# Performance work log

Hardware: AMD Instinct MI355X
Metric: run time of the kernel (lower is better)

## Reference

```python
import jax, jax.numpy as jnp
import numpy as np

BATCH, SEQ, DIM = 8, 2048, 512
NUM_Q, CODEBOOK = 8, 1024


def setup_inputs() -> dict:
    key = jax.random.key(0)
    k1, k2 = jax.random.split(key)
    x = jax.random.normal(k1, (BATCH, SEQ, DIM), dtype=jnp.float32)
    # one codebook per quantizer (uniform codebook size -> stacked [q, c, d])
    codebooks = jax.random.normal(k2, (NUM_Q, CODEBOOK, DIM), dtype=jnp.float32)
    return {"x": x, "codebooks": codebooks}


def reference(x, codebooks):
    """Residual VQ (Algorithm 1, SoundStream). Sequential nearest-neighbor
    quantization of the residual with straight-through estimator.
    project_in/project_out are Identity (codebook_dim == dim).
    Returns (quantized_out [b,n,d], indices [b,n,q], commit_losses [q]).
    """
    residual = x
    quantized_out = jnp.zeros_like(x)
    all_indices = []
    all_losses = []
    num_q = codebooks.shape[0]
    for q in range(num_q):  # small fixed loop over quantizer layers
        cb = codebooks[q]  # [c, d]
        # argmin of squared euclidean distance; ||r||^2 is constant over codes
        scores = -2.0 * jnp.einsum('bnd,cd->bnc', residual, cb) \
                 + jnp.sum(cb * cb, axis=-1)  # [b, n, c]
        idx = jnp.argmin(scores, axis=-1)  # [b, n]
        quant = cb[idx]  # gather codes: [b, n, d]
        # commitment loss (mse of detached quantize vs layer input)
        commit = jnp.mean((jax.lax.stop_gradient(quant) - residual) ** 2)
        # straight-through estimator
        quant_st = residual + jax.lax.stop_gradient(quant - residual)
        quantized_out = quantized_out + quant_st
        residual = residual - jax.lax.stop_gradient(quant)
        all_indices.append(idx)
        all_losses.append(commit)
    indices = jnp.stack(all_indices, axis=-1)  # [b, n, q]
    losses = jnp.stack(all_losses)  # [q]
    return quantized_out, indices, losses
```

## Files before the change

kernel.cpp:

```cpp
#include <hip/hip_runtime.h>
#include <cstdint>
#include <cstddef>


#define BATCH 8
#define SEQ   2048
#define DIM   512
#define NUMQ  8
#define CODES 1024
#define NPTS  (BATCH*SEQ)
#define MPTS  64
#define NWG   (NPTS/MPTS)
#define NTHR  512
#define NCHUNK 32
#define CHUNK_BYTES 32768

#define OUT_IDX   (BATCH*SEQ*DIM)
#define OUT_LOSS  (OUT_IDX + BATCH*SEQ*NUMQ)

#define WS_LOSS   0
#define WS_CNORM  1024
#define WS_CBH    40960
#define WS_CNORMD (WS_CBH + NUMQ*NCHUNK*CHUNK_BYTES)

typedef _Float16 f16x8  __attribute__((ext_vector_type(8)));
typedef _Float16 f16x4  __attribute__((ext_vector_type(4)));
typedef float    f32x16 __attribute__((ext_vector_type(16)));

__global__ void k_zero(double* loss) {
  if (threadIdx.x < NUMQ) loss[threadIdx.x] = 0.0;
}

__global__ void k_cnorm(const float* __restrict__ cb, float* __restrict__ cnorm) {
  int r = blockIdx.x * blockDim.x + threadIdx.x;
  const float* row = cb + (size_t)r * DIM;
  float s = 0.f;
  for (int d = 0; d < DIM; d += 4) {
    float4 v = *(const float4*)(row + d);
    s += v.x * v.x + v.y * v.y + v.z * v.z + v.w * v.w;
  }
  cnorm[r] = s;
}

__global__ void k_cnormd(const float* __restrict__ cb, double* __restrict__ cnd) {
  int r = blockIdx.x * blockDim.x + threadIdx.x;
  const float4* row = (const float4*)(cb + (size_t)r * DIM);
  double d0 = 0, d1 = 0, d2 = 0, d3 = 0;
  for (int i = 0; i < 128; i += 4) {
    float4 a = row[i], b = row[i + 1], c = row[i + 2], d = row[i + 3];
    d0 += (double)a.x * a.x + (double)a.y * a.y + (double)a.z * a.z + (double)a.w * a.w;
    d1 += (double)b.x * b.x + (double)b.y * b.y + (double)b.z * b.z + (double)b.w * b.w;
    d2 += (double)c.x * c.x + (double)c.y * c.y + (double)c.z * c.z + (double)c.w * c.w;
    d3 += (double)d.x * d.x + (double)d.y * d.y + (double)d.z * d.z + (double)d.w * d.w;
  }
  cnd[r] = (d0 + d1) + (d2 + d3);
}

__global__ void k_prep(const float* __restrict__ cb, unsigned char* __restrict__ cbH) {
  unsigned u = blockIdx.x * blockDim.x + threadIdx.x;
  unsigned h  = u & 1;
  unsigned v  = u >> 1;
  unsigned c  = v & 127;
  unsigned g  = (v >> 7) & 1;
  unsigned w  = (v >> 8) & 7;
  unsigned ks = (v >> 11) & 31;
  unsigned q  = v >> 16;
  unsigned code = (w << 7) | c;
  unsigned k = ks * 16 + g * 8 + h * 4;
  float4 val = *(const float4*)(cb + ((size_t)((q << 10) | code)) * DIM + k);
  f16x4 o;
  o[0] = (_Float16)val.x; o[1] = (_Float16)val.y;
  o[2] = (_Float16)val.z; o[3] = (_Float16)val.w;
  *(f16x4*)(cbH + (size_t)u * 8) = o;
}

struct BF { f16x8 b0, b1, b2, b3; };
__device__ __forceinline__ BF loadB(const unsigned char* __restrict__ p) {
  BF r;
  r.b0 = *(const f16x8*)(p);
  r.b1 = *(const f16x8*)(p + 512);
  r.b2 = *(const f16x8*)(p + 1024);
  r.b3 = *(const f16x8*)(p + 1536);
  return r;
}

__launch_bounds__(NTHR, 2)
__global__ void k_main(const float* __restrict__ x, const float* __restrict__ cb,
                       const unsigned char* __restrict__ cbH,
                       const float* __restrict__ cnorm,
                       const double* __restrict__ cnormd,
                       double* __restrict__ lossAcc,
                       float* __restrict__ out)
{
  __shared__ __align__(16) unsigned char Af[MPTS * DIM * 2];
  __shared__ float          s1w[MPTS][8];
  __shared__ unsigned short id1w[MPTS][8];
  __shared__ unsigned short cand[MPTS][8][4];
  __shared__ unsigned char  ccnt[MPTS][8];
  __shared__ float          gmA[MPTS];
  __shared__ int            win0A[MPTS];
  __shared__ unsigned short idxs[MPTS][NUMQ];
  __shared__ double         lred[8];

  const int tid = threadIdx.x;
  const int cl  = tid & 63;
  const int w   = tid >> 6;
  const int l31 = cl & 31;
  const int l5  = cl >> 5;
  const int wg  = blockIdx.x;

  const int rp = tid >> 3;
  const int rj = tid & 7;
  const size_t gp = (size_t)wg * MPTS + rp;
  float4 r4[16];
  {
    const float4* xr = (const float4*)(x + gp * DIM + rj * 64);
    #pragma unroll
    for (int i = 0; i < 16; ++i) r4[i] = xr[i];
  }

  for (int q = 0; q < NUMQ; ++q) {
    const unsigned char* bq = cbH + ((size_t)q << 20) + (w << 12) + (l5 << 11) + (l31 << 4);

    BF s0 = loadB(bq);
    BF s1 = loadB(bq + CHUNK_BYTES);

    #pragma unroll
    for (int i = 0; i < 8; ++i) {
      float4 a = r4[2 * i], b = r4[2 * i + 1];
      f16x8 v;
      v[0] = (_Float16)a.x; v[1] = (_Float16)a.y; v[2] = (_Float16)a.z; v[3] = (_Float16)a.w;
      v[4] = (_Float16)b.x; v[5] = (_Float16)b.y; v[6] = (_Float16)b.z; v[7] = (_Float16)b.w;
      int sl = ((i << 3) | rj) ^ (rp & 31);
      *(f16x8*)(Af + rp * 1024 + (sl << 4)) = v;
    }
    __syncthreads();

    f32x16 acc[2][4];
    #pragma unroll
    for (int mt = 0; mt < 2; ++mt)
      #pragma unroll
      for (int nt = 0; nt < 4; ++nt)
        #pragma unroll
        for (int e = 0; e < 16; ++e) acc[mt][nt][e] = 0.0f;

    #pragma unroll 1
    for (int kk = 0; kk < 16; ++kk) {
      const int ks = kk << 1;
      {
        const int s5 = (ks << 1) | l5;
        const int sf = ((((s5 & 7) << 3) | (s5 >> 3)) ^ l31) << 4;
        f16x8 a0 = *(const f16x8*)(Af + l31 * 1024 + sf);
        f16x8 a1 = *(const f16x8*)(Af + 32768 + l31 * 1024 + sf);
        __builtin_amdgcn_s_setprio(1);
        acc[0][0] = __builtin_amdgcn_mfma_f32_32x32x16_f16(a0, s0.b0, acc[0][0], 0, 0, 0);
        acc[0][1] = __builtin_amdgcn_mfma_f32_32x32x16_f16(a0, s0.b1, acc[0][1], 0, 0, 0);
        acc[0][2] = __builtin_amdgcn_mfma_f32_32x32x16_f16(a0, s0.b2, acc[0][2], 0, 0, 0);
        acc[0][3] = __builtin_amdgcn_mfma_f32_32x32x16_f16(a0, s0.b3, acc[0][3], 0, 0, 0);
        acc[1][0] = __builtin_amdgcn_mfma_f32_32x32x16_f16(a1, s0.b0, acc[1][0], 0, 0, 0);
        acc[1][1] = __builtin_amdgcn_mfma_f32_32x32x16_f16(a1, s0.b1, acc[1][1], 0, 0, 0);
        acc[1][2] = __builtin_amdgcn_mfma_f32_32x32x16_f16(a1, s0.b2, acc[1][2], 0, 0, 0);
        acc[1][3] = __builtin_amdgcn_mfma_f32_32x32x16_f16(a1, s0.b3, acc[1][3], 0, 0, 0);
        __builtin_amdgcn_s_setprio(0);
        if (ks + 2 < NCHUNK) s0 = loadB(bq + (size_t)(ks + 2) * CHUNK_BYTES);
      }
      {
        const int ks1 = ks + 1;
        const int s5 = (ks1 << 1) | l5;
        const int sf = ((((s5 & 7) << 3) | (s5 >> 3)) ^ l31) << 4;
        f16x8 a0 = *(const f16x8*)(Af + l31 * 1024 + sf);
        f16x8 a1 = *(const f16x8*)(Af + 32768 + l31 * 1024 + sf);
        __builtin_amdgcn_s_setprio(1);
        acc[0][0] = __builtin_amdgcn_mfma_f32_32x32x16_f16(a0, s1.b0, acc[0][0], 0, 0, 0);
        acc[0][1] = __builtin_amdgcn_mfma_f32_32x32x16_f16(a0, s1.b1, acc[0][1], 0, 0, 0);
        acc[0][2] = __builtin_amdgcn_mfma_f32_32x32x16_f16(a0, s1.b2, acc[0][2], 0, 0, 0);
        acc[0][3] = __builtin_amdgcn_mfma_f32_32x32x16_f16(a0, s1.b3, acc[0][3], 0, 0, 0);
        acc[1][0] = __builtin_amdgcn_mfma_f32_32x32x16_f16(a1, s1.b0, acc[1][0], 0, 0, 0);
        acc[1][1] = __builtin_amdgcn_mfma_f32_32x32x16_f16(a1, s1.b1, acc[1][1], 0, 0, 0);
        acc[1][2] = __builtin_amdgcn_mfma_f32_32x32x16_f16(a1, s1.b2, acc[1][2], 0, 0, 0);
        acc[1][3] = __builtin_amdgcn_mfma_f32_32x32x16_f16(a1, s1.b3, acc[1][3], 0, 0, 0);
        __builtin_amdgcn_s_setprio(0);
        if (ks1 + 2 < NCHUNK) s1 = loadB(bq + (size_t)(ks1 + 2) * CHUNK_BYTES);
      }
    }

    {
      const float* cnq = cnorm + (q << 10) + (w << 7) + l31;
      const float cn0 = cnq[0], cn1 = cnq[32], cn2 = cnq[64], cn3 = cnq[96];
      #pragma unroll
      for (int mt = 0; mt < 2; ++mt) {
        acc[mt][0] = acc[mt][0] * -2.0f + cn0;
        acc[mt][1] = acc[mt][1] * -2.0f + cn1;
        acc[mt][2] = acc[mt][2] * -2.0f + cn2;
        acc[mt][3] = acc[mt][3] * -2.0f + cn3;
      }
    }

    #pragma unroll
    for (int mt = 0; mt < 2; ++mt)
      #pragma unroll
      for (int r = 0; r < 16; ++r) {
        float s = acc[mt][0][r]; int bi = l31;
        if (acc[mt][1][r] < s) { s = acc[mt][1][r]; bi = 32 + l31; }
        if (acc[mt][2][r] < s) { s = acc[mt][2][r]; bi = 64 + l31; }
        if (acc[mt][3][r] < s) { s = acc[mt][3][r]; bi = 96 + l31; }
        float smin = s;
        #pragma unroll
        for (int m = 1; m < 32; m <<= 1) smin = fminf(smin, __shfl_xor(smin, m));
        unsigned long long bm = __ballot(s == smin);
        unsigned half = l5 ? (unsigned)(bm >> 32) : (unsigned)bm;
        int first = __builtin_ctz(half) + (l5 << 5);
        int id = __shfl(bi, first);
        if (l31 == 0) {
          int p = mt * 32 + (r & 3) + 8 * (r >> 2) + 4 * l5;
          s1w[p][w] = smin; id1w[p][w] = (unsigned short)id;
        }
      }
    __syncthreads();

    if (tid < MPTS) {
      int p = tid;
      float bs = s1w[p][0]; int bi = id1w[p][0];
      #pragma unroll
      for (int ww = 1; ww < 8; ++ww) {
        float s = s1w[p][ww];
        if (s < bs) { bs = s; bi = ww * 128 + id1w[p][ww]; }
      }
      gmA[p] = bs; win0A[p] = bi;
    }
    __syncthreads();

    #pragma unroll
    for (int mt = 0; mt < 2; ++mt)
      #pragma unroll
      for (int r = 0; r < 16; ++r) {
        const int p0 = mt * 32 + (r & 3) + 8 * (r >> 2);
        const float g0 = gmA[p0], g1 = gmA[p0 + 4];
        const float lim0 = g0 + 1.5f + 1e-4f * fabsf(g0);
        const float lim1 = g1 + 1.5f + 1e-4f * fabsf(g1);
        const float lim = l5 ? lim1 : lim0;
        unsigned long long b0 = __ballot(acc[mt][0][r] <= lim);
        unsigned long long b1 = __ballot(acc[mt][1][r] <= lim);
        unsigned long long b2 = __ballot(acc[mt][2][r] <= lim);
        unsigned long long b3 = __ballot(acc[mt][3][r] <= lim);
        if (cl == 0 || cl == 32) {
          const int p = p0 + (cl >> 3);
          unsigned short* cd = &cand[p][w][0];
          unsigned m0 = (cl == 0) ? (unsigned)b0 : (unsigned)(b0 >> 32);
          unsigned m1 = (cl == 0) ? (unsigned)b1 : (unsigned)(b1 >> 32);
          unsigned m2 = (cl == 0) ? (unsigned)b2 : (unsigned)(b2 >> 32);
          unsigned m3 = (cl == 0) ? (unsigned)b3 : (unsigned)(b3 >> 32);
          int n = 0;
          while (m0 && n < 4) { int bt = __builtin_ctz(m0); m0 &= m0 - 1; cd[n++] = (unsigned short)(bt); }
          while (m1 && n < 4) { int bt = __builtin_ctz(m1); m1 &= m1 - 1; cd[n++] = (unsigned short)(32 + bt); }
          while (m2 && n < 4) { int bt = __builtin_ctz(m2); m2 &= m2 - 1; cd[n++] = (unsigned short)(64 + bt); }
          while (m3 && n < 4) { int bt = __builtin_ctz(m3); m3 &= m3 - 1; cd[n++] = (unsigned short)(96 + bt); }
          ccnt[p][w] = (unsigned char)n;
        }
      }
    __syncthreads();

    {
      const int g  = cl >> 3;
      const int gl = cl & 7;
      const int p  = (w << 3) + g;
      int tot = 0;
      #pragma unroll
      for (int ww = 0; ww < 8; ++ww) tot += ccnt[p][ww];
      int winner = win0A[p];
      int mtot = tot;
      #pragma unroll
      for (int m = 1; m < 64; m <<= 1) { int o = __shfl_xor(mtot, m); if (o > mtot) mtot = o; }
      if (mtot > 1) {
        const size_t gpp = gp;
        double bs = 1.0e300, bs2 = 1.0e300; int bi = 0x7FFFFFFF;
        #pragma unroll 1
        for (int k = 0; k < mtot; ++k) {
          int cc = -1;
          if (tot > 1 && k < tot) {
            int rem = k, ww = 0;
            #pragma unroll 1
            for (; ww < 7; ++ww) { int nn = ccnt[p][ww]; if (rem < nn) break; rem -= nn; }
            cc = ww * 128 + cand[p][ww][rem];
          }
          double dt = 0.0;
          if (cc >= 0) {
            const float4* cr = (const float4*)(cb + ((size_t)q * CODES + cc) * DIM + gl * 64);
            double d0 = 0, d1 = 0, d2 = 0, d3 = 0;
            #pragma unroll
            for (int i = 0; i < 16; i += 4) {
              float4 c0 = cr[i], c1 = cr[i + 1], c2 = cr[i + 2], c3 = cr[i + 3];
              d0 += (double)r4[i].x * c0.x + (double)r4[i].y * c0.y
                  + (double)r4[i].z * c0.z + (double)r4[i].w * c0.w;
              d1 += (double)r4[i + 1].x * c1.x + (double)r4[i + 1].y * c1.y
                  + (double)r4[i + 1].z * c1.z + (double)r4[i + 1].w * c1.w;
              d2 += (double)r4[i + 2].x * c2.x + (double)r4[i + 2].y * c2.y
                  + (double)r4[i + 2].z * c2.z + (double)r4[i + 2].w * c2.w;
              d3 += (double)r4[i + 3].x * c3.x + (double)r4[i + 3].y * c3.y
                  + (double)r4[i + 3].z * c3.z + (double)r4[i + 3].w * c3.w;
            }
            dt = (d0 + d1) + (d2 + d3);
          }
          #pragma unroll
          for (int m = 1; m < 8; m <<= 1) dt += __shfl_xor(dt, m);
          if (cc >= 0) {
            double s = -2.0 * dt + cnormd[(q << 10) + cc];
            if (s < bs) { bs2 = bs; bs = s; bi = cc; }
            else if (s < bs2) { bs2 = s; }
          }
        }
        if (tot > 1 && bs2 - bs <= 1e-3 + 1e-6 * fabs(bs)) {
          bs = 1.0e300; bi = 0x7FFFFFFF;
          const float4* xr2 = (const float4*)(x + gpp * DIM + gl * 64);
          #pragma unroll 1
          for (int k = 0; k < tot; ++k) {
            int rem = k, ww = 0;
            #pragma unroll 1
            for (; ww < 7; ++ww) { int nn = ccnt[p][ww]; if (rem < nn) break; rem -= nn; }
            const int cc = ww * 128 + cand[p][ww][rem];
            const float4* cr = (const float4*)(cb + ((size_t)q * CODES + cc) * DIM + gl * 64);
            double dt = 0.0;
            #pragma unroll 1
            for (int i = 0; i < 16; ++i) {
              float4 xv = xr2[i];
              double rhx = xv.x, rhy = xv.y, rhz = xv.z, rhw = xv.w;
              #pragma unroll 1
              for (int t2 = 0; t2 < q; ++t2) {
                const float4* qr = (const float4*)(cb + ((size_t)t2 * CODES + idxs[p][t2]) * DIM + gl * 64);
                float4 qv = qr[i];
                rhx -= (double)qv.x; rhy -= (double)qv.y;
                rhz -= (double)qv.z; rhw -= (double)qv.w;
              }
              float4 cv = cr[i];
              dt += rhx * cv.x + rhy * cv.y + rhz * cv.z + rhw * cv.w;
            }
            #pragma unroll
            for (int m = 1; m < 8; m <<= 1) dt += __shfl_xor(dt, m);
            double s = -2.0 * dt + cnormd[(q << 10) + cc];
            if (s < bs || (s == bs && cc < bi)) { bs = s; bi = cc; }
          }
        }
        if (tot > 1) winner = bi;
      }
      if (gl == 0) idxs[p][q] = (unsigned short)winner;
    }
    __syncthreads();

    {
      const int win = idxs[rp][q];
      const float4* cr = (const float4*)(cb + ((size_t)q * CODES + win) * DIM + rj * 64);
      double ls0 = 0.0, ls1 = 0.0;
      #pragma unroll
      for (int i = 0; i < 16; i += 2) {
        float4 c0 = cr[i], c1 = cr[i + 1];
        float dx0 = c0.x - r4[i].x, dy0 = c0.y - r4[i].y;
        float dz0 = c0.z - r4[i].z, dw0 = c0.w - r4[i].w;
        ls0 += (double)dx0 * dx0 + (double)dy0 * dy0 + (double)dz0 * dz0 + (double)dw0 * dw0;
        r4[i].x -= c0.x; r4[i].y -= c0.y; r4[i].z -= c0.z; r4[i].w -= c0.w;
        float dx1 = c1.x - r4[i + 1].x, dy1 = c1.y - r4[i + 1].y;
        float dz1 = c1.z - r4[i + 1].z, dw1 = c1.w - r4[i + 1].w;
        ls1 += (double)dx1 * dx1 + (double)dy1 * dy1 + (double)dz1 * dz1 + (double)dw1 * dw1;
        r4[i + 1].x -= c1.x; r4[i + 1].y -= c1.y; r4[i + 1].z -= c1.z; r4[i + 1].w -= c1.w;
      }
      double ls = ls0 + ls1;
      #pragma unroll
      for (int m = 1; m < 64; m <<= 1) ls += __shfl_xor(ls, m);
      if (cl == 0) lred[w] = ls;
      __syncthreads();
      if (tid == 0) {
        double t = lred[0] + lred[1] + lred[2] + lred[3]
                 + lred[4] + lred[5] + lred[6] + lred[7];
        atomicAdd(lossAcc + q, t);
      }
      __syncthreads();
    }
  }

  {
    const float4* xr = (const float4*)(x + gp * DIM + rj * 64);
    float4* orow = (float4*)(out + gp * DIM + rj * 64);
    #pragma unroll
    for (int i = 0; i < 16; ++i) {
      float4 xv = xr[i];
      float4 o;
      o.x = xv.x - r4[i].x; o.y = xv.y - r4[i].y;
      o.z = xv.z - r4[i].z; o.w = xv.w - r4[i].w;
      orow[i] = o;
    }
  }
  if (tid < MPTS) {
    float* ob = out + OUT_IDX + ((size_t)wg * MPTS + tid) * NUMQ;
    #pragma unroll
    for (int j = 0; j < NUMQ; ++j) ob[j] = (float)idxs[tid][j];
  }
}

__global__ void k_fin(const double* __restrict__ loss, float* __restrict__ out) {
  int t = threadIdx.x;
  if (t < NUMQ)
    out[OUT_LOSS + t] = (float)(loss[t] / (double)((size_t)BATCH * SEQ * DIM));
}

extern "C" void kernel_launch(void* const* d_in, const int* in_sizes, int n_in,
                              void* d_out, int out_size, void* d_ws, size_t ws_size,
                              hipStream_t stream) {
  (void)in_sizes; (void)n_in; (void)out_size; (void)ws_size;
  const float* x  = (const float*)d_in[0];
  const float* cb = (const float*)d_in[1];
  float* out = (float*)d_out;
  char* ws = (char*)d_ws;
  double* loss = (double*)(ws + WS_LOSS);
  float* cnorm = (float*)(ws + WS_CNORM);
  unsigned char* cbH = (unsigned char*)(ws + WS_CBH);
  double* cnormd = (double*)(ws + WS_CNORMD);

  k_zero<<<1, 64, 0, stream>>>(loss);
  k_cnorm<<<NUMQ * CODES / 256, 256, 0, stream>>>(cb, cnorm);
  k_cnormd<<<NUMQ * CODES / 256, 256, 0, stream>>>(cb, cnormd);
  k_prep<<<NUMQ * NCHUNK * CHUNK_BYTES / 8 / 256, 256, 0, stream>>>(cb, cbH);
  k_main<<<NWG, NTHR, 0, stream>>>(x, cb, cbH, cnorm, cnormd, loss, out);
  k_fin<<<1, 64, 0, stream>>>(loss, out);
}
```

Baseline: 543.1 us.

## Split codebook scan into two halves to cut accumulator registers and prefetch across quantizers

```diff
diff --git a/kernel.cpp b/kernel.cpp
--- a/kernel.cpp
+++ b/kernel.cpp
@@ -74,13 +74,11 @@
   *(f16x4*)(cbH + (size_t)u * 8) = o;
 }
 
-struct BF { f16x8 b0, b1, b2, b3; };
-__device__ __forceinline__ BF loadB(const unsigned char* __restrict__ p) {
-  BF r;
+struct BF2 { f16x8 b0, b1; };
+__device__ __forceinline__ BF2 loadB2(const unsigned char* __restrict__ p) {
+  BF2 r;
   r.b0 = *(const f16x8*)(p);
   r.b1 = *(const f16x8*)(p + 512);
-  r.b2 = *(const f16x8*)(p + 1024);
-  r.b3 = *(const f16x8*)(p + 1536);
   return r;
 }
 
@@ -93,12 +91,12 @@
                        float* __restrict__ out)
 {
   __shared__ __align__(16) unsigned char Af[MPTS * DIM * 2];
-  __shared__ float          s1w[MPTS][8];
-  __shared__ unsigned short id1w[MPTS][8];
-  __shared__ unsigned short cand[MPTS][8][4];
-  __shared__ unsigned char  ccnt[MPTS][8];
-  __shared__ float          gmA[MPTS];
-  __shared__ int            win0A[MPTS];
+  __shared__ float          s1w[MPTS][16];
+  __shared__ unsigned short id1w[MPTS][16];
+  __shared__ unsigned short cand[MPTS][2][8][4];
+  __shared__ unsigned char  ccnt[MPTS][2][8];
+  __shared__ float          gmH[MPTS][2];
+  __shared__ unsigned short win2[MPTS][2];
   __shared__ unsigned short idxs[MPTS][NUMQ];
   __shared__ double         lred[8];
 
@@ -119,12 +117,15 @@
     for (int i = 0; i < 16; ++i) r4[i] = xr[i];
   }
 
+  const int laneOff = (l5 << 11) + ((((w & 1) << 6) + l31) << 4);
+  const size_t segW = ((size_t)(w >> 1)) << 12;
+
+  #define SEGBASE(q_, h_) (cbH + ((size_t)(q_) << 20) + (((size_t)(h_) << 14)) + segW + laneOff)
+
+  BF2 s0 = loadB2(SEGBASE(0, 0));
+  BF2 s1 = loadB2(SEGBASE(0, 0) + CHUNK_BYTES);
+
   for (int q = 0; q < NUMQ; ++q) {
-    const unsigned char* bq = cbH + ((size_t)q << 20) + (w << 12) + (l5 << 11) + (l31 << 4);
-
-    BF s0 = loadB(bq);
-    BF s1 = loadB(bq + CHUNK_BYTES);
-
     #pragma unroll
     for (int i = 0; i < 8; ++i) {
       float4 a = r4[2 * i], b = r4[2 * i + 1];
@@ -136,129 +137,129 @@
     }
     __syncthreads();
 
-    f32x16 acc[2][4];
-    #pragma unroll
-    for (int mt = 0; mt < 2; ++mt)
-      #pragma unroll
-      for (int nt = 0; nt < 4; ++nt)
+    #pragma unroll 1
+    for (int h = 0; h < 2; ++h) {
+      const unsigned char* bh = SEGBASE(q, h);
+      const unsigned char* bnext =
+          (h == 0) ? SEGBASE(q, 1)
+                   : ((q + 1 < NUMQ) ? SEGBASE(q + 1, 0) : nullptr);
+
+      f32x16 acc[2][2];
+      #pragma unroll
+      for (int mt = 0; mt < 2; ++mt)
         #pragma unroll
-        for (int e = 0; e < 16; ++e) acc[mt][nt][e] = 0.0f;
-
-    #pragma unroll 1
-    for (int kk = 0; kk < 16; ++kk) {
-      const int ks = kk << 1;
+        for (int nt = 0; nt < 2; ++nt)
+          #pragma unroll
+          for (int e = 0; e < 16; ++e) acc[mt][nt][e] = 0.0f;
+
+      #pragma unroll 1
+      for (int kk = 0; kk < 16; ++kk) {
+        const int ks = kk << 1;
+        {
+          const int s5 = (ks << 1) | l5;
+          const int sf = ((((s5 & 7) << 3) | (s5 >> 3)) ^ l31) << 4;
+          f16x8 a0 = *(const f16x8*)(Af + l31 * 1024 + sf);
+          f16x8 a1 = *(const f16x8*)(Af + 32768 + l31 * 1024 + sf);
+          __builtin_amdgcn_s_setprio(1);
+          acc[0][0] = __builtin_amdgcn_mfma_f32_32x32x16_f16(a0, s0.b0, acc[0][0], 0, 0, 0);
+          acc[0][1] = __builtin_amdgcn_mfma_f32_32x32x16_f16(a0, s0.b1, acc[0][1], 0, 0, 0);
+          acc[1][0] = __builtin_amdgcn_mfma_f32_32x32x16_f16(a1, s0.b0, acc[1][0], 0, 0, 0);
+          acc[1][1] = __builtin_amdgcn_mfma_f32_32x32x16_f16(a1, s0.b1, acc[1][1], 0, 0, 0);
+          __builtin_amdgcn_s_setprio(0);
+          const int n2 = ks + 2;
+          const unsigned char* pf =
+              (n2 < NCHUNK) ? bh + (size_t)n2 * CHUNK_BYTES
+                            : (bnext ? bnext + (size_t)(n2 - NCHUNK) * CHUNK_BYTES : nullptr);
+          if (pf) s0 = loadB2(pf);
+        }
+        {
+          const int ks1 = ks + 1;
+          const int s5 = (ks1 << 1) | l5;
+          const int sf = ((((s5 & 7) << 3) | (s5 >> 3)) ^ l31) << 4;
+          f16x8 a0 = *(const f16x8*)(Af + l31 * 1024 + sf);
+          f16x8 a1 = *(const f16x8*)(Af + 32768 + l31 * 1024 + sf);
+          __builtin_amdgcn_s_setprio(1);
+          acc[0][0] = __builtin_amdgcn_mfma_f32_32x32x16_f16(a0, s1.b0, acc[0][0], 0, 0, 0);
+          acc[0][1] = __builtin_amdgcn_mfma_f32_32x32x16_f16(a0, s1.b1, acc[0][1], 0, 0, 0);
+          acc[1][0] = __builtin_amdgcn_mfma_f32_32x32x16_f16(a1, s1.b0, acc[1][0], 0, 0, 0);
+          acc[1][1] = __builtin_amdgcn_mfma_f32_32x32x16_f16(a1, s1.b1, acc[1][1], 0, 0, 0);
+          __builtin_amdgcn_s_setprio(0);
+          const int n3 = ks1 + 2;
+          const unsigned char* pf =
+              (n3 < NCHUNK) ? bh + (size_t)n3 * CHUNK_BYTES
+                            : (bnext ? bnext + (size_t)(n3 - NCHUNK) * CHUNK_BYTES : nullptr);
+          if (pf) s1 = loadB2(pf);
+        }
+      }
+
       {
-        const int s5 = (ks << 1) | l5;
-        const int sf = ((((s5 & 7) << 3) | (s5 >> 3)) ^ l31) << 4;
-        f16x8 a0 = *(const f16x8*)(Af + l31 * 1024 + sf);
-        f16x8 a1 = *(const f16x8*)(Af + 32768 + l31 * 1024 + sf);
-        __builtin_amdgcn_s_setprio(1);
-        acc[0][0] = __builtin_amdgcn_mfma_f32_32x32x16_f16(a0, s0.b0, acc[0][0], 0, 0, 0);
-        acc[0][1] = __builtin_amdgcn_mfma_f32_32x32x16_f16(a0, s0.b1, acc[0][1], 0, 0, 0);
-        acc[0][2] = __builtin_amdgcn_mfma_f32_32x32x16_f16(a0, s0.b2, acc[0][2], 0, 0, 0);
-        acc[0][3] = __builtin_amdgcn_mfma_f32_32x32x16_f16(a0, s0.b3, acc[0][3], 0, 0, 0);
-        acc[1][0] = __builtin_amdgcn_mfma_f32_32x32x16_f16(a1, s0.b0, acc[1][0], 0, 0, 0);
-        acc[1][1] = __builtin_amdgcn_mfma_f32_32x32x16_f16(a1, s0.b1, acc[1][1], 0, 0, 0);
-        acc[1][2] = __builtin_amdgcn_mfma_f32_32x32x16_f16(a1, s0.b2, acc[1][2], 0, 0, 0);
-        acc[1][3] = __builtin_amdgcn_mfma_f32_32x32x16_f16(a1, s0.b3, acc[1][3], 0, 0, 0);
-        __builtin_amdgcn_s_setprio(0);
-        if (ks + 2 < NCHUNK) s0 = loadB(bq + (size_t)(ks + 2) * CHUNK_BYTES);
-      }
-      {
-        const int ks1 = ks + 1;
-        const int s5 = (ks1 << 1) | l5;
-        const int sf = ((((s5 & 7) << 3) | (s5 >> 3)) ^ l31) << 4;
-        f16x8 a0 = *(const f16x8*)(Af + l31 * 1024 + sf);
-        f16x8 a1 = *(const f16x8*)(Af + 32768 + l31 * 1024 + sf);
-        __builtin_amdgcn_s_setprio(1);
-        acc[0][0] = __builtin_amdgcn_mfma_f32_32x32x16_f16(a0, s1.b0, acc[0][0], 0, 0, 0);
-        acc[0][1] = __builtin_amdgcn_mfma_f32_32x32x16_f16(a0, s1.b1, acc[0][1], 0, 0, 0);
-        acc[0][2] = __builtin_amdgcn_mfma_f32_32x32x16_f16(a0, s1.b2, acc[0][2], 0, 0, 0);
-        acc[0][3] = __builtin_amdgcn_mfma_f32_32x32x16_f16(a0, s1.b3, acc[0][3], 0, 0, 0);
-        acc[1][0] = __builtin_amdgcn_mfma_f32_32x32x16_f16(a1, s1.b0, acc[1][0], 0, 0, 0);
-        acc[1][1] = __builtin_amdgcn_mfma_f32_32x32x16_f16(a1, s1.b1, acc[1][1], 0, 0, 0);
-        acc[1][2] = __builtin_amdgcn_mfma_f32_32x32x16_f16(a1, s1.b2, acc[1][2], 0, 0, 0);
-        acc[1][3] = __builtin_amdgcn_mfma_f32_32x32x16_f16(a1, s1.b3, acc[1][3], 0, 0, 0);
-        __builtin_amdgcn_s_setprio(0);
-        if (ks1 + 2 < NCHUNK) s1 = loadB(bq + (size_t)(ks1 + 2) * CHUNK_BYTES);
-      }
+        const float* cnq = cnorm + (q << 10) + (h << 9) + (w << 6) + l31;
+        const float cn0 = cnq[0], cn1 = cnq[32];
+        #pragma unroll
+        for (int mt = 0; mt < 2; ++mt) {
+          acc[mt][0] = acc[mt][0] * -2.0f + cn0;
+          acc[mt][1] = acc[mt][1] * -2.0f + cn1;
+        }
+      }
+
+      const int hw = (h << 3) | w;
+      #pragma unroll
+      for (int mt = 0; mt < 2; ++mt)
+        #pragma unroll
+        for (int r = 0; r < 16; ++r) {
+          float s = acc[mt][0][r]; int bi = l31;
+          if (acc[mt][1][r] < s) { s = acc[mt][1][r]; bi = 32 + l31; }
+          float smin = s;
+          #pragma unroll
+          for (int m = 1; m < 32; m <<= 1) smin = fminf(smin, __shfl_xor(smin, m));
+          unsigned long long bm = __ballot(s == smin);
+          unsigned half = l5 ? (unsigned)(bm >> 32) : (unsigned)bm;
+          int first = __builtin_ctz(half) + (l5 << 5);
+          int id = __shfl(bi, first);
+          if (l31 == 0) {
+            int p = mt * 32 + (r & 3) + 8 * (r >> 2) + 4 * l5;
+            s1w[p][hw] = smin; id1w[p][hw] = (unsigned short)id;
+          }
+        }
+      __syncthreads();
+
+      if (tid < MPTS) {
+        int p = tid;
+        float bs = s1w[p][(h << 3)]; int bw = 0;
+        #pragma unroll
+        for (int ww = 1; ww < 8; ++ww) {
+          float s = s1w[p][(h << 3) | ww];
+          if (s < bs) { bs = s; bw = ww; }
+        }
+        gmH[p][h] = bs;
+        win2[p][h] = (unsigned short)((h << 9) + (bw << 6) + id1w[p][(h << 3) | bw]);
+      }
+      __syncthreads();
+
+      #pragma unroll
+      for (int mt = 0; mt < 2; ++mt)
+        #pragma unroll
+        for (int r = 0; r < 16; ++r) {
+          const int p0 = mt * 32 + (r & 3) + 8 * (r >> 2);
+          const float g0 = gmH[p0][h], g1 = gmH[p0 + 4][h];
+          const float lim0 = g0 + 1.5f + 1e-4f * fabsf(g0);
+          const float lim1 = g1 + 1.5f + 1e-4f * fabsf(g1);
+          const float lim = l5 ? lim1 : lim0;
+          unsigned long long b0 = __ballot(acc[mt][0][r] <= lim);
+          unsigned long long b1 = __ballot(acc[mt][1][r] <= lim);
+          if (cl == 0 || cl == 32) {
+            const int p = p0 + (cl >> 3);
+            unsigned short* cd = &cand[p][h][w][0];
+            unsigned m0 = (cl == 0) ? (unsigned)b0 : (unsigned)(b0 >> 32);
+            unsigned m1 = (cl == 0) ? (unsigned)b1 : (unsigned)(b1 >> 32);
+            int n = 0;
+            while (m0 && n < 4) { int bt = __builtin_ctz(m0); m0 &= m0 - 1; cd[n++] = (unsigned short)bt; }
+            while (m1 && n < 4) { int bt = __builtin_ctz(m1); m1 &= m1 - 1; cd[n++] = (unsigned short)(32 + bt); }
+            ccnt[p][h][w] = (unsigned char)n;
+          }
+        }
+      __syncthreads();
     }
-
-    {
-      const float* cnq = cnorm + (q << 10) + (w << 7) + l31;
-      const float cn0 = cnq[0], cn1 = cnq[32], cn2 = cnq[64], cn3 = cnq[96];
-      #pragma unroll
-      for (int mt = 0; mt < 2; ++mt) {
-        acc[mt][0] = acc[mt][0] * -2.0f + cn0;
-        acc[mt][1] = acc[mt][1] * -2.0f + cn1;
-        acc[mt][2] = acc[mt][2] * -2.0f + cn2;
-        acc[mt][3] = acc[mt][3] * -2.0f + cn3;
-      }
-    }
-
-    #pragma unroll
-    for (int mt = 0; mt < 2; ++mt)
-      #pragma unroll
-      for (int r = 0; r < 16; ++r) {
-        float s = acc[mt][0][r]; int bi = l31;
-        if (acc[mt][1][r] < s) { s = acc[mt][1][r]; bi = 32 + l31; }
-        if (acc[mt][2][r] < s) { s = acc[mt][2][r]; bi = 64 + l31; }
-        if (acc[mt][3][r] < s) { s = acc[mt][3][r]; bi = 96 + l31; }
-        float smin = s;
-        #pragma unroll
-        for (int m = 1; m < 32; m <<= 1) smin = fminf(smin, __shfl_xor(smin, m));
-        unsigned long long bm = __ballot(s == smin);
-        unsigned half = l5 ? (unsigned)(bm >> 32) : (unsigned)bm;
-        int first = __builtin_ctz(half) + (l5 << 5);
-        int id = __shfl(bi, first);
-        if (l31 == 0) {
-          int p = mt * 32 + (r & 3) + 8 * (r >> 2) + 4 * l5;
-          s1w[p][w] = smin; id1w[p][w] = (unsigned short)id;
-        }
-      }
-    __syncthreads();
-
-    if (tid < MPTS) {
-      int p = tid;
-      float bs = s1w[p][0]; int bi = id1w[p][0];
-      #pragma unroll
-      for (int ww = 1; ww < 8; ++ww) {
-        float s = s1w[p][ww];
-        if (s < bs) { bs = s; bi = ww * 128 + id1w[p][ww]; }
-      }
-      gmA[p] = bs; win0A[p] = bi;
-    }
-    __syncthreads();
-
-    #pragma unroll
-    for (int mt = 0; mt < 2; ++mt)
-      #pragma unroll
-      for (int r = 0; r < 16; ++r) {
-        const int p0 = mt * 32 + (r & 3) + 8 * (r >> 2);
-        const float g0 = gmA[p0], g1 = gmA[p0 + 4];
-        const float lim0 = g0 + 1.5f + 1e-4f * fabsf(g0);
-        const float lim1 = g1 + 1.5f + 1e-4f * fabsf(g1);
-        const float lim = l5 ? lim1 : lim0;
-        unsigned long long b0 = __ballot(acc[mt][0][r] <= lim);
-        unsigned long long b1 = __ballot(acc[mt][1][r] <= lim);
-        unsigned long long b2 = __ballot(acc[mt][2][r] <= lim);
-        unsigned long long b3 = __ballot(acc[mt][3][r] <= lim);
-        if (cl == 0 || cl == 32) {
-          const int p = p0 + (cl >> 3);
-          unsigned short* cd = &cand[p][w][0];
-          unsigned m0 = (cl == 0) ? (unsigned)b0 : (unsigned)(b0 >> 32);
-          unsigned m1 = (cl == 0) ? (unsigned)b1 : (unsigned)(b1 >> 32);
-          unsigned m2 = (cl == 0) ? (unsigned)b2 : (unsigned)(b2 >> 32);
-          unsigned m3 = (cl == 0) ? (unsigned)b3 : (unsigned)(b3 >> 32);
-          int n = 0;
-          while (m0 && n < 4) { int bt = __builtin_ctz(m0); m0 &= m0 - 1; cd[n++] = (unsigned short)(bt); }
-          while (m1 && n < 4) { int bt = __builtin_ctz(m1); m1 &= m1 - 1; cd[n++] = (unsigned short)(32 + bt); }
-          while (m2 && n < 4) { int bt = __builtin_ctz(m2); m2 &= m2 - 1; cd[n++] = (unsigned short)(64 + bt); }
-          while (m3 && n < 4) { int bt = __builtin_ctz(m3); m3 &= m3 - 1; cd[n++] = (unsigned short)(96 + bt); }
-          ccnt[p][w] = (unsigned char)n;
-        }
-      }
-    __syncthreads();
 
     {
       const int g  = cl >> 3;
@@ -266,22 +267,28 @@
       const int p  = (w << 3) + g;
       int tot = 0;
       #pragma unroll
-      for (int ww = 0; ww < 8; ++ww) tot += ccnt[p][ww];
-      int winner = win0A[p];
+      for (int s = 0; s < 16; ++s) tot += ccnt[p][s >> 3][s & 7];
+      int winner;
+      {
+        float g0 = gmH[p][0], g1 = gmH[p][1];
+        winner = (g0 <= g1) ? win2[p][0] : win2[p][1];
+      }
       int mtot = tot;
       #pragma unroll
       for (int m = 1; m < 64; m <<= 1) { int o = __shfl_xor(mtot, m); if (o > mtot) mtot = o; }
       if (mtot > 1) {
-        const size_t gpp = gp;
         double bs = 1.0e300, bs2 = 1.0e300; int bi = 0x7FFFFFFF;
         #pragma unroll 1
         for (int k = 0; k < mtot; ++k) {
           int cc = -1;
           if (tot > 1 && k < tot) {
-            int rem = k, ww = 0;
+            int rem = k, slot = 0;
             #pragma unroll 1
-            for (; ww < 7; ++ww) { int nn = ccnt[p][ww]; if (rem < nn) break; rem -= nn; }
-            cc = ww * 128 + cand[p][ww][rem];
+            for (; slot < 15; ++slot) {
+              int nn = ccnt[p][slot >> 3][slot & 7];
+              if (rem < nn) break; rem -= nn;
+            }
+            cc = ((slot >> 3) << 9) + ((slot & 7) << 6) + cand[p][slot >> 3][slot & 7][rem];
           }
           double dt = 0.0;
           if (cc >= 0) {
@@ -311,13 +318,16 @@
         }
         if (tot > 1 && bs2 - bs <= 1e-3 + 1e-6 * fabs(bs)) {
           bs = 1.0e300; bi = 0x7FFFFFFF;
-          const float4* xr2 = (const float4*)(x + gpp * DIM + gl * 64);
+          const float4* xr2 = (const float4*)(x + gp * DIM + gl * 64);
           #pragma unroll 1
           for (int k = 0; k < tot; ++k) {
-            int rem = k, ww = 0;
+            int rem = k, slot = 0;
             #pragma unroll 1
-            for (; ww < 7; ++ww) { int nn = ccnt[p][ww]; if (rem < nn) break; rem -= nn; }
-            const int cc = ww * 128 + cand[p][ww][rem];
+            for (; slot < 15; ++slot) {
+              int nn = ccnt[p][slot >> 3][slot & 7];
+              if (rem < nn) break; rem -= nn;
+            }
+            const int cc = ((slot >> 3) << 9) + ((slot & 7) << 6) + cand[p][slot >> 3][slot & 7][rem];
             const float4* cr = (const float4*)(cb + ((size_t)q * CODES + cc) * DIM + gl * 64);
             double dt = 0.0;
             #pragma unroll 1
```

After: 688.0 us. 26.7% more time.

## Triple-buffer codebook fragment prefetch across quantizers and fold candidate threshold pass

Applied to the files above, without the earlier changes.

```diff
diff --git a/kernel.cpp b/kernel.cpp
--- a/kernel.cpp
+++ b/kernel.cpp
@@ -13,6 +13,7 @@
 #define NWG   (NPTS/MPTS)
 #define NTHR  512
 #define NCHUNK 32
+#define NCHUNK_TOT (NUMQ*NCHUNK)
 #define CHUNK_BYTES 32768
 
 #define OUT_IDX   (BATCH*SEQ*DIM)
@@ -97,7 +98,6 @@
   __shared__ unsigned short id1w[MPTS][8];
   __shared__ unsigned short cand[MPTS][8][4];
   __shared__ unsigned char  ccnt[MPTS][8];
-  __shared__ float          gmA[MPTS];
   __shared__ int            win0A[MPTS];
   __shared__ unsigned short idxs[MPTS][NUMQ];
   __shared__ double         lred[8];
@@ -119,12 +119,13 @@
     for (int i = 0; i < 16; ++i) r4[i] = xr[i];
   }
 
+  const unsigned char* base = cbH + (w << 12) + (l5 << 11) + (l31 << 4);
+
+  BF s0 = loadB(base);
+  BF s1 = loadB(base + (size_t)1 * CHUNK_BYTES);
+  BF s2 = loadB(base + (size_t)2 * CHUNK_BYTES);
+
   for (int q = 0; q < NUMQ; ++q) {
-    const unsigned char* bq = cbH + ((size_t)q << 20) + (w << 12) + (l5 << 11) + (l31 << 4);
-
-    BF s0 = loadB(bq);
-    BF s1 = loadB(bq + CHUNK_BYTES);
-
     #pragma unroll
     for (int i = 0; i < 8; ++i) {
       float4 a = r4[2 * i], b = r4[2 * i + 1];
@@ -144,44 +145,46 @@
         #pragma unroll
         for (int e = 0; e < 16; ++e) acc[mt][nt][e] = 0.0f;
 
-    #pragma unroll 1
-    for (int kk = 0; kk < 16; ++kk) {
-      const int ks = kk << 1;
-      {
-        const int s5 = (ks << 1) | l5;
-        const int sf = ((((s5 & 7) << 3) | (s5 >> 3)) ^ l31) << 4;
-        f16x8 a0 = *(const f16x8*)(Af + l31 * 1024 + sf);
-        f16x8 a1 = *(const f16x8*)(Af + 32768 + l31 * 1024 + sf);
-        __builtin_amdgcn_s_setprio(1);
-        acc[0][0] = __builtin_amdgcn_mfma_f32_32x32x16_f16(a0, s0.b0, acc[0][0], 0, 0, 0);
-        acc[0][1] = __builtin_amdgcn_mfma_f32_32x32x16_f16(a0, s0.b1, acc[0][1], 0, 0, 0);
-        acc[0][2] = __builtin_amdgcn_mfma_f32_32x32x16_f16(a0, s0.b2, acc[0][2], 0, 0, 0);
-        acc[0][3] = __builtin_amdgcn_mfma_f32_32x32x16_f16(a0, s0.b3, acc[0][3], 0, 0, 0);
-        acc[1][0] = __builtin_amdgcn_mfma_f32_32x32x16_f16(a1, s0.b0, acc[1][0], 0, 0, 0);
-        acc[1][1] = __builtin_amdgcn_mfma_f32_32x32x16_f16(a1, s0.b1, acc[1][1], 0, 0, 0);
-        acc[1][2] = __builtin_amdgcn_mfma_f32_32x32x16_f16(a1, s0.b2, acc[1][2], 0, 0, 0);
-        acc[1][3] = __builtin_amdgcn_mfma_f32_32x32x16_f16(a1, s0.b3, acc[1][3], 0, 0, 0);
-        __builtin_amdgcn_s_setprio(0);
-        if (ks + 2 < NCHUNK) s0 = loadB(bq + (size_t)(ks + 2) * CHUNK_BYTES);
-      }
-      {
-        const int ks1 = ks + 1;
-        const int s5 = (ks1 << 1) | l5;
-        const int sf = ((((s5 & 7) << 3) | (s5 >> 3)) ^ l31) << 4;
-        f16x8 a0 = *(const f16x8*)(Af + l31 * 1024 + sf);
-        f16x8 a1 = *(const f16x8*)(Af + 32768 + l31 * 1024 + sf);
-        __builtin_amdgcn_s_setprio(1);
-        acc[0][0] = __builtin_amdgcn_mfma_f32_32x32x16_f16(a0, s1.b0, acc[0][0], 0, 0, 0);
-        acc[0][1] = __builtin_amdgcn_mfma_f32_32x32x16_f16(a0, s1.b1, acc[0][1], 0, 0, 0);
-        acc[0][2] = __builtin_amdgcn_mfma_f32_32x32x16_f16(a0, s1.b2, acc[0][2], 0, 0, 0);
-        acc[0][3] = __builtin_amdgcn_mfma_f32_32x32x16_f16(a0, s1.b3, acc[0][3], 0, 0, 0);
-        acc[1][0] = __builtin_amdgcn_mfma_f32_32x32x16_f16(a1, s1.b0, acc[1][0], 0, 0, 0);
-        acc[1][1] = __builtin_amdgcn_mfma_f32_32x32x16_f16(a1, s1.b1, acc[1][1], 0, 0, 0);
-        acc[1][2] = __builtin_amdgcn_mfma_f32_32x32x16_f16(a1, s1.b2, acc[1][2], 0, 0, 0);
-        acc[1][3] = __builtin_amdgcn_mfma_f32_32x32x16_f16(a1, s1.b3, acc[1][3], 0, 0, 0);
-        __builtin_amdgcn_s_setprio(0);
-        if (ks1 + 2 < NCHUNK) s1 = loadB(bq + (size_t)(ks1 + 2) * CHUNK_BYTES);
-      }
+    auto sub = [&](int ks, BF& S) {
+      const int s5 = (ks << 1) | l5;
+      const int sf = ((((s5 & 7) << 3) | (s5 >> 3)) ^ l31) << 4;
+      f16x8 a0 = *(const f16x8*)(Af + l31 * 1024 + sf);
+      f16x8 a1 = *(const f16x8*)(Af + 32768 + l31 * 1024 + sf);
+      __builtin_amdgcn_s_setprio(1);
+      acc[0][0] = __builtin_amdgcn_mfma_f32_32x32x16_f16(a0, S.b0, acc[0][0], 0, 0, 0);
+      acc[0][1] = __builtin_amdgcn_mfma_f32_32x32x16_f16(a0, S.b1, acc[0][1], 0, 0, 0);
+      acc[0][2] = __builtin_amdgcn_mfma_f32_32x32x16_f16(a0, S.b2, acc[0][2], 0, 0, 0);
+      acc[0][3] = __builtin_amdgcn_mfma_f32_32x32x16_f16(a0, S.b3, acc[0][3], 0, 0, 0);
+      acc[1][0] = __builtin_amdgcn_mfma_f32_32x32x16_f16(a1, S.b0, acc[1][0], 0, 0, 0);
+      acc[1][1] = __builtin_amdgcn_mfma_f32_32x32x16_f16(a1, S.b1, acc[1][1], 0, 0, 0);
+      acc[1][2] = __builtin_amdgcn_mfma_f32_32x32x16_f16(a1, S.b2, acc[1][2], 0, 0, 0);
+      acc[1][3] = __builtin_amdgcn_mfma_f32_32x32x16_f16(a1, S.b3, acc[1][3], 0, 0, 0);
+      __builtin_amdgcn_s_setprio(0);
+    };
+
+    auto kphase = [&](BF& A, BF& B, BF& C) {
+      const int g0 = q << 5;
+      #pragma unroll 1
+      for (int kk = 0; kk < 30; kk += 3) {
+        sub(kk, A);
+        A = loadB(base + (size_t)(g0 + kk + 3) * CHUNK_BYTES);
+        sub(kk + 1, B);
+        B = loadB(base + (size_t)(g0 + kk + 4) * CHUNK_BYTES);
+        sub(kk + 2, C);
+        { const int gid = g0 + kk + 5;
+          if (gid < NCHUNK_TOT) C = loadB(base + (size_t)gid * CHUNK_BYTES); }
+      }
+      sub(30, A);
+      { const int gid = g0 + 33;
+        if (gid < NCHUNK_TOT) A = loadB(base + (size_t)gid * CHUNK_BYTES); }
+      sub(31, B);
+      { const int gid = g0 + 34;
+        if (gid < NCHUNK_TOT) B = loadB(base + (size_t)gid * CHUNK_BYTES); }
+    };
+    switch (q % 3) {
+      case 0: kphase(s0, s1, s2); break;
+      case 1: kphase(s2, s0, s1); break;
+      default: kphase(s1, s2, s0); break;
     }
 
     {
@@ -208,43 +211,17 @@
         #pragma unroll
         for (int m = 1; m < 32; m <<= 1) smin = fminf(smin, __shfl_xor(smin, m));
         unsigned long long bm = __ballot(s == smin);
-        unsigned half = l5 ? (unsigned)(bm >> 32) : (unsigned)bm;
-        int first = __builtin_ctz(half) + (l5 << 5);
+        unsigned halfm = l5 ? (unsigned)(bm >> 32) : (unsigned)bm;
+        int first = __builtin_ctz(halfm) + (l5 << 5);
         int id = __shfl(bi, first);
-        if (l31 == 0) {
-          int p = mt * 32 + (r & 3) + 8 * (r >> 2) + 4 * l5;
-          s1w[p][w] = smin; id1w[p][w] = (unsigned short)id;
-        }
-      }
-    __syncthreads();
-
-    if (tid < MPTS) {
-      int p = tid;
-      float bs = s1w[p][0]; int bi = id1w[p][0];
-      #pragma unroll
-      for (int ww = 1; ww < 8; ++ww) {
-        float s = s1w[p][ww];
-        if (s < bs) { bs = s; bi = ww * 128 + id1w[p][ww]; }
-      }
-      gmA[p] = bs; win0A[p] = bi;
-    }
-    __syncthreads();
-
-    #pragma unroll
-    for (int mt = 0; mt < 2; ++mt)
-      #pragma unroll
-      for (int r = 0; r < 16; ++r) {
-        const int p0 = mt * 32 + (r & 3) + 8 * (r >> 2);
-        const float g0 = gmA[p0], g1 = gmA[p0 + 4];
-        const float lim0 = g0 + 1.5f + 1e-4f * fabsf(g0);
-        const float lim1 = g1 + 1.5f + 1e-4f * fabsf(g1);
-        const float lim = l5 ? lim1 : lim0;
+        const float lim = smin + 1.5f + 1e-4f * fabsf(smin);
         unsigned long long b0 = __ballot(acc[mt][0][r] <= lim);
         unsigned long long b1 = __ballot(acc[mt][1][r] <= lim);
         unsigned long long b2 = __ballot(acc[mt][2][r] <= lim);
         unsigned long long b3 = __ballot(acc[mt][3][r] <= lim);
-        if (cl == 0 || cl == 32) {
-          const int p = p0 + (cl >> 3);
+        if (l31 == 0) {
+          const int p = mt * 32 + (r & 3) + 8 * (r >> 2) + 4 * l5;
+          s1w[p][w] = smin; id1w[p][w] = (unsigned short)id;
           unsigned short* cd = &cand[p][w][0];
           unsigned m0 = (cl == 0) ? (unsigned)b0 : (unsigned)(b0 >> 32);
           unsigned m1 = (cl == 0) ? (unsigned)b1 : (unsigned)(b1 >> 32);
@@ -260,6 +237,18 @@
       }
     __syncthreads();
 
+    if (tid < MPTS) {
+      int p = tid;
+      float bs = s1w[p][0]; int bi = id1w[p][0];
+      #pragma unroll
+      for (int ww = 1; ww < 8; ++ww) {
+        float s = s1w[p][ww];
+        if (s < bs) { bs = s; bi = ww * 128 + id1w[p][ww]; }
+      }
+      win0A[p] = bi;
+    }
+    __syncthreads();
+
     {
       const int g  = cl >> 3;
       const int gl = cl & 7;
@@ -272,7 +261,6 @@
       #pragma unroll
       for (int m = 1; m < 64; m <<= 1) { int o = __shfl_xor(mtot, m); if (o > mtot) mtot = o; }
       if (mtot > 1) {
-        const size_t gpp = gp;
         double bs = 1.0e300, bs2 = 1.0e300; int bi = 0x7FFFFFFF;
         #pragma unroll 1
         for (int k = 0; k < mtot; ++k) {
@@ -311,7 +299,7 @@
         }
         if (tot > 1 && bs2 - bs <= 1e-3 + 1e-6 * fabs(bs)) {
           bs = 1.0e300; bi = 0x7FFFFFFF;
-          const float4* xr2 = (const float4*)(x + gpp * DIM + gl * 64);
+          const float4* xr2 = (const float4*)(x + gp * DIM + gl * 64);
           #pragma unroll 1
           for (int k = 0; k < tot; ++k) {
             int rem = k, ww = 0;
```

New measurement: 1.004 ms. +84.9%, slower.

## Fuse setup kernels, drop block-wide argmin syncs, finalize loss in main kernel

Applied to the files above, without the earlier changes.

```diff
diff --git a/kernel.cpp b/kernel.cpp
--- a/kernel.cpp
+++ b/kernel.cpp
@@ -22,56 +22,52 @@
 #define WS_CNORM  1024
 #define WS_CBH    40960
 #define WS_CNORMD (WS_CBH + NUMQ*NCHUNK*CHUNK_BYTES)
+#define WS_DONE   (WS_CNORMD + 8192*8)
 
 typedef _Float16 f16x8  __attribute__((ext_vector_type(8)));
 typedef _Float16 f16x4  __attribute__((ext_vector_type(4)));
 typedef float    f32x16 __attribute__((ext_vector_type(16)));
 
-__global__ void k_zero(double* loss) {
-  if (threadIdx.x < NUMQ) loss[threadIdx.x] = 0.0;
-}
-
-__global__ void k_cnorm(const float* __restrict__ cb, float* __restrict__ cnorm) {
-  int r = blockIdx.x * blockDim.x + threadIdx.x;
-  const float* row = cb + (size_t)r * DIM;
-  float s = 0.f;
-  for (int d = 0; d < DIM; d += 4) {
-    float4 v = *(const float4*)(row + d);
-    s += v.x * v.x + v.y * v.y + v.z * v.z + v.w * v.w;
-  }
-  cnorm[r] = s;
-}
-
-__global__ void k_cnormd(const float* __restrict__ cb, double* __restrict__ cnd) {
-  int r = blockIdx.x * blockDim.x + threadIdx.x;
-  const float4* row = (const float4*)(cb + (size_t)r * DIM);
-  double d0 = 0, d1 = 0, d2 = 0, d3 = 0;
-  for (int i = 0; i < 128; i += 4) {
-    float4 a = row[i], b = row[i + 1], c = row[i + 2], d = row[i + 3];
-    d0 += (double)a.x * a.x + (double)a.y * a.y + (double)a.z * a.z + (double)a.w * a.w;
-    d1 += (double)b.x * b.x + (double)b.y * b.y + (double)b.z * b.z + (double)b.w * b.w;
-    d2 += (double)c.x * c.x + (double)c.y * c.y + (double)c.z * c.z + (double)c.w * c.w;
-    d3 += (double)d.x * d.x + (double)d.y * d.y + (double)d.z * d.z + (double)d.w * d.w;
-  }
-  cnd[r] = (d0 + d1) + (d2 + d3);
-}
-
-__global__ void k_prep(const float* __restrict__ cb, unsigned char* __restrict__ cbH) {
+__global__ void k_prep(const float* __restrict__ cb, unsigned char* __restrict__ cbH,
+                       float* __restrict__ cnorm, double* __restrict__ cnd,
+                       double* __restrict__ loss, unsigned* __restrict__ done) {
   unsigned u = blockIdx.x * blockDim.x + threadIdx.x;
-  unsigned h  = u & 1;
-  unsigned v  = u >> 1;
-  unsigned c  = v & 127;
-  unsigned g  = (v >> 7) & 1;
-  unsigned w  = (v >> 8) & 7;
-  unsigned ks = (v >> 11) & 31;
-  unsigned q  = v >> 16;
-  unsigned code = (w << 7) | c;
-  unsigned k = ks * 16 + g * 8 + h * 4;
-  float4 val = *(const float4*)(cb + ((size_t)((q << 10) | code)) * DIM + k);
-  f16x4 o;
-  o[0] = (_Float16)val.x; o[1] = (_Float16)val.y;
-  o[2] = (_Float16)val.z; o[3] = (_Float16)val.w;
-  *(f16x4*)(cbH + (size_t)u * 8) = o;
+  {
+    unsigned h  = u & 1;
+    unsigned v  = u >> 1;
+    unsigned c  = v & 127;
+    unsigned g  = (v >> 7) & 1;
+    unsigned w  = (v >> 8) & 7;
+    unsigned ks = (v >> 11) & 31;
+    unsigned q  = v >> 16;
+    unsigned code = (w << 7) | c;
+    unsigned k = ks * 16 + g * 8 + h * 4;
+    float4 val = *(const float4*)(cb + ((size_t)((q << 10) | code)) * DIM + k);
+    f16x4 o;
+    o[0] = (_Float16)val.x; o[1] = (_Float16)val.y;
+    o[2] = (_Float16)val.z; o[3] = (_Float16)val.w;
+    *(f16x4*)(cbH + (size_t)u * 8) = o;
+  }
+  if (u < NUMQ) loss[u] = 0.0;
+  if (u == NUMQ) *done = 0u;
+  if (u < NUMQ * CODES) {
+    const float4* row = (const float4*)(cb + (size_t)u * DIM);
+    float s = 0.f;
+    double d0 = 0, d1 = 0, d2 = 0, d3 = 0;
+    for (int i = 0; i < 128; i += 4) {
+      float4 a = row[i], b = row[i + 1], c2 = row[i + 2], d = row[i + 3];
+      s += a.x * a.x + a.y * a.y + a.z * a.z + a.w * a.w
+         + b.x * b.x + b.y * b.y + b.z * b.z + b.w * b.w
+         + c2.x * c2.x + c2.y * c2.y + c2.z * c2.z + c2.w * c2.w
+         + d.x * d.x + d.y * d.y + d.z * d.z + d.w * d.w;
+      d0 += (double)a.x * a.x + (double)a.y * a.y + (double)a.z * a.z + (double)a.w * a.w;
+      d1 += (double)b.x * b.x + (double)b.y * b.y + (double)b.z * b.z + (double)b.w * b.w;
+      d2 += (double)c2.x * c2.x + (double)c2.y * c2.y + (double)c2.z * c2.z + (double)c2.w * c2.w;
+      d3 += (double)d.x * d.x + (double)d.y * d.y + (double)d.z * d.z + (double)d.w * d.w;
+    }
+    cnorm[u] = s;
+    cnd[u] = (d0 + d1) + (d2 + d3);
+  }
 }
 
 struct BF { f16x8 b0, b1, b2, b3; };
@@ -90,6 +86,7 @@
                        const float* __restrict__ cnorm,
                        const double* __restrict__ cnormd,
                        double* __restrict__ lossAcc,
+                       unsigned* __restrict__ done,
                        float* __restrict__ out)
 {
   __shared__ __align__(16) unsigned char Af[MPTS * DIM * 2];
@@ -97,8 +94,6 @@
   __shared__ unsigned short id1w[MPTS][8];
   __shared__ unsigned short cand[MPTS][8][4];
   __shared__ unsigned char  ccnt[MPTS][8];
-  __shared__ float          gmA[MPTS];
-  __shared__ int            win0A[MPTS];
   __shared__ unsigned short idxs[MPTS][NUMQ];
   __shared__ double         lred[8];
 
@@ -208,43 +203,17 @@
         #pragma unroll
         for (int m = 1; m < 32; m <<= 1) smin = fminf(smin, __shfl_xor(smin, m));
         unsigned long long bm = __ballot(s == smin);
-        unsigned half = l5 ? (unsigned)(bm >> 32) : (unsigned)bm;
-        int first = __builtin_ctz(half) + (l5 << 5);
+        unsigned halfm = l5 ? (unsigned)(bm >> 32) : (unsigned)bm;
+        int first = __builtin_ctz(halfm) + (l5 << 5);
         int id = __shfl(bi, first);
-        if (l31 == 0) {
-          int p = mt * 32 + (r & 3) + 8 * (r >> 2) + 4 * l5;
-          s1w[p][w] = smin; id1w[p][w] = (unsigned short)id;
-        }
-      }
-    __syncthreads();
-
-    if (tid < MPTS) {
-      int p = tid;
-      float bs = s1w[p][0]; int bi = id1w[p][0];
-      #pragma unroll
-      for (int ww = 1; ww < 8; ++ww) {
-        float s = s1w[p][ww];
-        if (s < bs) { bs = s; bi = ww * 128 + id1w[p][ww]; }
-      }
-      gmA[p] = bs; win0A[p] = bi;
-    }
-    __syncthreads();
-
-    #pragma unroll
-    for (int mt = 0; mt < 2; ++mt)
-      #pragma unroll
-      for (int r = 0; r < 16; ++r) {
-        const int p0 = mt * 32 + (r & 3) + 8 * (r >> 2);
-        const float g0 = gmA[p0], g1 = gmA[p0 + 4];
-        const float lim0 = g0 + 1.5f + 1e-4f * fabsf(g0);
-        const float lim1 = g1 + 1.5f + 1e-4f * fabsf(g1);
-        const float lim = l5 ? lim1 : lim0;
+        const float lim = smin + 1.5f + 1e-4f * fabsf(smin);
         unsigned long long b0 = __ballot(acc[mt][0][r] <= lim);
         unsigned long long b1 = __ballot(acc[mt][1][r] <= lim);
         unsigned long long b2 = __ballot(acc[mt][2][r] <= lim);
         unsigned long long b3 = __ballot(acc[mt][3][r] <= lim);
-        if (cl == 0 || cl == 32) {
-          const int p = p0 + (cl >> 3);
+        if (l31 == 0) {
+          const int p = mt * 32 + (r & 3) + 8 * (r >> 2) + 4 * l5;
+          s1w[p][w] = smin; id1w[p][w] = (unsigned short)id;
           unsigned short* cd = &cand[p][w][0];
           unsigned m0 = (cl == 0) ? (unsigned)b0 : (unsigned)(b0 >> 32);
           unsigned m1 = (cl == 0) ? (unsigned)b1 : (unsigned)(b1 >> 32);
@@ -264,15 +233,23 @@
       const int g  = cl >> 3;
       const int gl = cl & 7;
       const int p  = (w << 3) + g;
+      float bs0 = s1w[p][gl]; int bw = gl; int bid = id1w[p][gl];
+      #pragma unroll
+      for (int m = 1; m < 8; m <<= 1) {
+        float os = __shfl_xor(bs0, m);
+        int ow = __shfl_xor(bw, m);
+        int oid = __shfl_xor(bid, m);
+        if (os < bs0 || (os == bs0 && ow < bw)) { bs0 = os; bw = ow; bid = oid; }
+      }
+      int winner = bw * 128 + bid;
+
       int tot = 0;
       #pragma unroll
       for (int ww = 0; ww < 8; ++ww) tot += ccnt[p][ww];
-      int winner = win0A[p];
       int mtot = tot;
       #pragma unroll
       for (int m = 1; m < 64; m <<= 1) { int o = __shfl_xor(mtot, m); if (o > mtot) mtot = o; }
       if (mtot > 1) {
-        const size_t gpp = gp;
         double bs = 1.0e300, bs2 = 1.0e300; int bi = 0x7FFFFFFF;
         #pragma unroll 1
         for (int k = 0; k < mtot; ++k) {
@@ -311,7 +288,7 @@
         }
         if (tot > 1 && bs2 - bs <= 1e-3 + 1e-6 * fabs(bs)) {
           bs = 1.0e300; bi = 0x7FFFFFFF;
-          const float4* xr2 = (const float4*)(x + gpp * DIM + gl * 64);
+          const float4* xr2 = (const float4*)(x + gp * DIM + gl * 64);
           #pragma unroll 1
           for (int k = 0; k < tot; ++k) {
             int rem = k, ww = 0;
@@ -393,12 +370,18 @@
     #pragma unroll
     for (int j = 0; j < NUMQ; ++j) ob[j] = (float)idxs[tid][j];
   }
-}
-
-__global__ void k_fin(const double* __restrict__ loss, float* __restrict__ out) {
-  int t = threadIdx.x;
-  if (t < NUMQ)
-    out[OUT_LOSS + t] = (float)(loss[t] / (double)((size_t)BATCH * SEQ * DIM));
+
+  __threadfence();
+  if (tid == 0) {
+    unsigned old = atomicAdd(done, 1u);
+    if (old == (unsigned)(NWG - 1)) {
+      #pragma unroll
+      for (int t = 0; t < NUMQ; ++t) {
+        double v = atomicAdd(lossAcc + t, 0.0);
+        out[OUT_LOSS + t] = (float)(v / (double)((size_t)BATCH * SEQ * DIM));
+      }
+    }
+  }
 }
 
 extern "C" void kernel_launch(void* const* d_in, const int* in_sizes, int n_in,
@@ -413,11 +396,9 @@
   float* cnorm = (float*)(ws + WS_CNORM);
   unsigned char* cbH = (unsigned char*)(ws + WS_CBH);
   double* cnormd = (double*)(ws + WS_CNORMD);
-
-  k_zero<<<1, 64, 0, stream>>>(loss);
-  k_cnorm<<<NUMQ * CODES / 256, 256, 0, stream>>>(cb, cnorm);
-  k_cnormd<<<NUMQ * CODES / 256, 256, 0, stream>>>(cb, cnormd);
-  k_prep<<<NUMQ * NCHUNK * CHUNK_BYTES / 8 / 256, 256, 0, stream>>>(cb, cbH);
-  k_main<<<NWG, NTHR, 0, stream>>>(x, cb, cbH, cnorm, cnormd, loss, out);
-  k_fin<<<1, 64, 0, stream>>>(loss, out);
+  unsigned* done = (unsigned*)(ws + WS_DONE);
+
+  k_prep<<<NUMQ * NCHUNK * CHUNK_BYTES / 8 / 256, 256, 0, stream>>>(
+      cb, cbH, cnorm, cnormd, loss, done);
+  k_main<<<NWG, NTHR, 0, stream>>>(x, cb, cbH, cnorm, cnormd, loss, done, out);
 }
```

After: 1.003 ms. +84.6%, slower.
